# Performance work log

Hardware: AMD Instinct MI355X
Metric: run time of the kernel (lower is better)

Reference implementation:

```python
import jax, jax.numpy as jnp
import numpy as np
import math

NUM_CLASSES = 15
IN_CH = 256
FEAT_CH = 256
STRIDES = (8, 16, 32, 64, 128)
SCALES = (4.0,)
RATIOS = (6.0,)
ANGLES = (-0.125 * math.pi, 0.125 * math.pi, 0.375 * math.pi, 0.625 * math.pi)
NUM_ANCHORS = len(SCALES) * len(RATIOS) * len(ANGLES)  # 4
WH_RATIO_CLIP = 1e-6


def conv2d(x, w, b, pad):
    y = jax.lax.conv_general_dilated(
        x, w, window_strides=(1, 1), padding=[(pad, pad), (pad, pad)],
        dimension_numbers=("NCHW", "OIHW", "NCHW"))
    return y + b[None, :, None, None]


def gen_grid_anchors(base_size, feat_h, feat_w, stride):
    # AnchorGeneratorRotated (S2ANet style): base anchors [A,5] = (xc,yc,w,h,angle)
    scales = jnp.asarray(SCALES, jnp.float32)
    ratios = jnp.asarray(RATIOS, jnp.float32)
    angles = jnp.asarray(ANGLES, jnp.float32)
    h_ratios = jnp.sqrt(ratios)
    w_ratios = 1.0 / h_ratios
    ones = jnp.ones_like(angles)
    ws = (base_size * w_ratios[:, None, None] * scales[None, :, None] * ones[None, None, :]).reshape(-1)
    hs = (base_size * h_ratios[:, None, None] * scales[None, :, None] * ones[None, None, :]).reshape(-1)
    ang = jnp.tile(angles, ratios.size * scales.size)
    ctr = 0.5 * (base_size - 1.0)
    base = jnp.stack([jnp.full_like(ws, ctr), jnp.full_like(ws, ctr), ws, hs, ang], axis=-1)  # [A,5]
    xx = jnp.arange(feat_w, dtype=jnp.float32) * stride
    yy = jnp.arange(feat_h, dtype=jnp.float32) * stride
    gx, gy = jnp.meshgrid(xx, yy)  # [H,W]
    zeros = jnp.zeros_like(gx)
    shift = jnp.stack([gx, gy, zeros, zeros, zeros], axis=-1)  # [H,W,5]
    return base[None, None] + shift[:, :, None, :]  # [H,W,A,5]


def norm_angle(a):
    # normalize to [-pi/4, 3pi/4)
    return (a + 0.25 * jnp.pi) % jnp.pi - 0.25 * jnp.pi


def rboxes_decode(anchors, deltas):
    # is_encode_relative=False branch of delta2rbox
    max_ratio = abs(math.log(WH_RATIO_CLIP))
    dx, dy, dw, dh, da = jnp.split(deltas, 5, axis=-1)
    rx, ry, rw, rh, ra = jnp.split(anchors, 5, axis=-1)
    dw = jnp.clip(dw, -max_ratio, max_ratio)
    dh = jnp.clip(dh, -max_ratio, max_ratio)
    gx = dx * rw + rx
    gy = dy * rh + ry
    gw = rw * jnp.exp(dw)
    gh = rh * jnp.exp(dh)
    ga = norm_angle(da + ra)
    return jnp.concatenate([gx, gy, gw, gh, ga], axis=-1)


def _head_level(x, stride, p):
    B, _, H, W = x.shape
    # reg tower (2 stacked 3x3 conv + relu)
    r = jax.nn.relu(conv2d(x, p["reg_w0"], p["reg_b0"], 1))
    r = jax.nn.relu(conv2d(r, p["reg_w1"], p["reg_b1"], 1))
    bbox = conv2d(r, p["reg_head_w"], p["reg_head_b"], 0)
    bbox = bbox.transpose(0, 2, 3, 1).reshape(B, H, W, NUM_ANCHORS, 5)
    conf = conv2d(r, p["conf_w"], p["conf_b"], 0)
    conf = conf.transpose(0, 2, 3, 1).reshape(B, H, W, NUM_ANCHORS, 1)
    anchors = gen_grid_anchors(float(stride), H, W, float(stride))  # [H,W,A,5]
    dec = rboxes_decode(anchors[None], jax.lax.stop_gradient(bbox))  # [B,H,W,A,5]
    # refine-anchor selection: pick decoded box of max-confidence anchor per location
    conf_sig = jax.nn.sigmoid(jax.lax.stop_gradient(conf))[..., 0]  # [B,H,W,A]
    idx = jnp.argmax(conf_sig, axis=3)  # [B,H,W]
    refine = jnp.take_along_axis(dec, idx[..., None, None], axis=3)[:, :, :, 0, :]  # [B,H,W,5]
    # cls tower
    c = jax.nn.relu(conv2d(x, p["cls_w0"], p["cls_b0"], 1))
    c = jax.nn.relu(conv2d(c, p["cls_w1"], p["cls_b1"], 1))
    cls = conv2d(c, p["cls_head_w"], p["cls_head_b"], 0)
    cls = cls.transpose(0, 2, 3, 1).reshape(B, H, W, NUM_ANCHORS, NUM_CLASSES)
    # per-image scores as in get_bboxes: sigmoid(cls) * sigmoid(conf)
    scores = jax.nn.sigmoid(cls.reshape(B, -1, NUM_CLASSES)) * jax.nn.sigmoid(conf.reshape(B, -1, 1))
    return scores, dec.reshape(B, -1, 5), refine


def setup_inputs() -> dict:
    key = jax.random.key(0)
    ks = jax.random.split(key, 24)
    B = 8
    sizes = [(128, 128), (64, 64), (32, 32), (16, 16), (8, 8)]
    inp = {}
    for i, (h, w) in enumerate(sizes):
        inp[f"feat{i}"] = jax.random.normal(ks[i], (B, IN_CH, h, w), jnp.float32)
    std = 0.01
    bias_cls = float(-np.log((1 - 0.01) / 0.01))
    inp["reg_w0"] = jax.random.normal(ks[5], (FEAT_CH, IN_CH, 3, 3), jnp.float32) * std
    inp["reg_b0"] = jnp.zeros((FEAT_CH,), jnp.float32)
    inp["reg_w1"] = jax.random.normal(ks[6], (FEAT_CH, FEAT_CH, 3, 3), jnp.float32) * std
    inp["reg_b1"] = jnp.zeros((FEAT_CH,), jnp.float32)
    inp["cls_w0"] = jax.random.normal(ks[7], (FEAT_CH, IN_CH, 3, 3), jnp.float32) * std
    inp["cls_b0"] = jnp.zeros((FEAT_CH,), jnp.float32)
    inp["cls_w1"] = jax.random.normal(ks[8], (FEAT_CH, FEAT_CH, 3, 3), jnp.float32) * std
    inp["cls_b1"] = jnp.zeros((FEAT_CH,), jnp.float32)
    inp["reg_head_w"] = jax.random.normal(ks[9], (5 * NUM_ANCHORS, FEAT_CH, 1, 1), jnp.float32) * std
    inp["reg_head_b"] = jnp.zeros((5 * NUM_ANCHORS,), jnp.float32)
    inp["cls_head_w"] = jax.random.normal(ks[10], (NUM_CLASSES * NUM_ANCHORS, FEAT_CH, 1, 1), jnp.float32) * std
    inp["cls_head_b"] = jnp.full((NUM_CLASSES * NUM_ANCHORS,), bias_cls, jnp.float32)
    inp["conf_w"] = jax.random.normal(ks[11], (NUM_ANCHORS, FEAT_CH, 1, 1), jnp.float32) * std
    inp["conf_b"] = jnp.full((NUM_ANCHORS,), bias_cls, jnp.float32)
    return inp


def reference(feat0, feat1, feat2, feat3, feat4,
              reg_w0, reg_b0, reg_w1, reg_b1,
              cls_w0, cls_b0, cls_w1, cls_b1,
              reg_head_w, reg_head_b, cls_head_w, cls_head_b,
              conf_w, conf_b):
    p = dict(reg_w0=reg_w0, reg_b0=reg_b0, reg_w1=reg_w1, reg_b1=reg_b1,
             cls_w0=cls_w0, cls_b0=cls_b0, cls_w1=cls_w1, cls_b1=cls_b1,
             reg_head_w=reg_head_w, reg_head_b=reg_head_b,
             cls_head_w=cls_head_w, cls_head_b=cls_head_b,
             conf_w=conf_w, conf_b=conf_b)
    feats = [feat0, feat1, feat2, feat3, feat4]
    scores_ls, boxes_ls = [], []
    for x, s in zip(feats, STRIDES):
        sc, bx, _ = _head_level(x, s, p)
        scores_ls.append(sc)
        boxes_ls.append(bx)
    scores = jnp.concatenate(scores_ls, axis=1)  # [B, N_total, num_classes]
    boxes = jnp.concatenate(boxes_ls, axis=1)    # [B, N_total, 5]
    return scores, boxes
```

## Files before the change

kernel.cpp:

```cpp
#include <hip/hip_runtime.h>


typedef __attribute__((ext_vector_type(8))) _Float16 f16x8;
typedef __attribute__((ext_vector_type(4))) float f32x4;

#define SCORES_TOTAL 10475520ull

__device__ __forceinline__ unsigned short f2h(float f) {
  union { _Float16 h; unsigned short u; } x;
  x.h = (_Float16)f;
  return x.u;
}

__device__ __forceinline__ float sigmf(float x) {
  return 1.0f / (1.0f + expf(-x));
}

__device__ __forceinline__ void gload_lds16(const unsigned short* g,
                                            unsigned short* l) {
  __builtin_amdgcn_global_load_lds(
      (const __attribute__((address_space(1))) unsigned int*)g,
      (__attribute__((address_space(3))) unsigned int*)l, 16, 0, 0);
}

__device__ __forceinline__ void lvl_lookup(int gm, int& logW, int& mbase) {
  if (gm < 131072) { logW = 7; mbase = 0; }
  else if (gm < 163840) { logW = 6; mbase = 131072; }
  else if (gm < 172032) { logW = 5; mbase = 163840; }
  else if (gm < 174080) { logW = 4; mbase = 172032; }
  else { logW = 3; mbase = 174080; }
}

__global__ __launch_bounds__(256) void prep_convw(
    const float* __restrict__ w0, const float* __restrict__ w1,
    const float* __restrict__ w2, const float* __restrict__ w3,
    unsigned short* __restrict__ wtout) {
  int g = blockIdx.x * 256 + threadIdx.x;
  int q = g >> 16;
  int wsel = q / 9;
  int kk = q - wsel * 9;
  int r = g & 65535;
  int oc = r >> 8, ic = r & 255;
  const float* src = (wsel == 0) ? w0 : (wsel == 1) ? w1 : (wsel == 2) ? w2 : w3;
  float v = src[(size_t)(oc * 256 + ic) * 9 + kk];
  wtout[(size_t)wsel * 589824 + (size_t)((kk << 8) + oc) * 256 + ic] = f2h(v);
}

__global__ __launch_bounds__(256) void prep_small(
    const float* __restrict__ clsh, const float* __restrict__ regh,
    const float* __restrict__ confw,
    unsigned short* __restrict__ wc, unsigned short* __restrict__ wh,
    unsigned short* __restrict__ zp) {
  int g = blockIdx.x * 256 + threadIdx.x;
  if (g < 16384) {
    int row = g >> 8, ic = g & 255;
    float v = (row < 60) ? clsh[row * 256 + ic] : 0.0f;
    wc[g] = f2h(v);
  } else if (g < 24576) {
    int gg = g - 16384;
    int row = gg >> 8, ic = gg & 255;
    float v = 0.0f;
    if (row < 20) v = regh[row * 256 + ic];
    else if (row < 24) v = confw[(row - 20) * 256 + ic];
    wh[gg] = f2h(v);
  } else if (g < 24640) {
    zp[g - 24576] = 0;
  }
}

__global__ __launch_bounds__(256) void to_nhwc_all(
    const float* __restrict__ f0, const float* __restrict__ f1,
    const float* __restrict__ f2, const float* __restrict__ f3,
    const float* __restrict__ f4, unsigned short* __restrict__ out) {
  __shared__ unsigned short L[64][258];
  const int t = threadIdx.x;
  const int gm0 = blockIdx.x * 64;
  int logW, mbase;
  const float* in;
  if (gm0 < 131072) { logW = 7; mbase = 0; in = f0; }
  else if (gm0 < 163840) { logW = 6; mbase = 131072; in = f1; }
  else if (gm0 < 172032) { logW = 5; mbase = 163840; in = f2; }
  else if (gm0 < 174080) { logW = 4; mbase = 172032; in = f3; }
  else { logW = 3; mbase = 174080; in = f4; }
  const int logHW = 2 * logW;
  const int HW = 1 << logHW;
  const int lm0 = gm0 - mbase;
  const int b = lm0 >> logHW;
  const int hw0 = lm0 & (HW - 1);
#pragma unroll
  for (int it = 0; it < 16; ++it) {
    int c = it * 16 + (t >> 4);
    int j4 = (t & 15) * 4;
    float4 v = *reinterpret_cast<const float4*>(
        in + (size_t)(b * 256 + c) * HW + hw0 + j4);
    L[j4 + 0][c] = f2h(v.x);
    L[j4 + 1][c] = f2h(v.y);
    L[j4 + 2][c] = f2h(v.z);
    L[j4 + 3][c] = f2h(v.w);
  }
  __syncthreads();
#pragma unroll
  for (int it = 0; it < 16; ++it) {
    int j = it * 4 + (t >> 6);
    int c4 = (t & 63) * 4;
    unsigned v0 = (unsigned)L[j][c4 + 0] | ((unsigned)L[j][c4 + 1] << 16);
    unsigned v1 = (unsigned)L[j][c4 + 2] | ((unsigned)L[j][c4 + 3] << 16);
    uint2 v = make_uint2(v0, v1);
    *reinterpret_cast<uint2*>(out + ((size_t)(gm0 + j) << 8) + c4) = v;
  }
}

template <int LOGW>
__global__ __launch_bounds__(512, 2) void conv256p(
    const unsigned short* __restrict__ xin,
    const unsigned short* __restrict__ wt,
    const float* __restrict__ bias,
    const unsigned short* __restrict__ zp,
    unsigned short* __restrict__ yout,
    int gm_base) {
  __shared__ unsigned short pool[65536];
  const int t = threadIdx.x;
  const int lane = t & 63;
  const int wv = t >> 6;
  const int wm = wv >> 2;
  const int wn = wv & 3;
  const int gm0 = gm_base + blockIdx.x * 256;
  int logW, mbase;
  if constexpr (LOGW > 0) {
    logW = LOGW;
    mbase = 0;
  } else {
    lvl_lookup(gm0, logW, mbase);
  }
  const int H = 1 << logW, W = H;
  const int logHW = 2 * logW;
  const int HWm1 = (1 << logHW) - 1, Wm1 = W - 1;

  const int schk = ((lane & 3) ^ ((lane >> 3) & 3)) << 3;
  const unsigned short* aptr[2];
  const unsigned short* bptr[2];
  int amsk[2];
#pragma unroll
  for (int j = 0; j < 2; ++j) {
    int r = (wv << 5) + (j << 4) + (lane >> 2);
    int gm = gm0 + r;
    int lm = gm - mbase;
    int hw = lm & HWm1;
    int hj = hw >> logW, wj = hw & Wm1;
    aptr[j] = xin + ((size_t)gm << 8) + schk;
    bptr[j] = wt + ((size_t)r << 8) + schk;
    bool hm = hj > 0, hp = hj < H - 1, wlo = wj > 0, whi = wj < W - 1;
    int m = 0;
#pragma unroll
    for (int kk = 0; kk < 9; ++kk) {
      int dy = kk / 3 - 1, dxv = kk % 3 - 1;
      bool ok = (dy < 0 ? hm : (dy > 0 ? hp : true)) &&
                (dxv < 0 ? wlo : (dxv > 0 ? whi : true));
      m |= (ok ? 1 : 0) << kk;
    }
    amsk[j] = m;
  }
  const int sdstA = (wv << 10) + ((lane >> 6) << 9);

  f32x4 acc[8][4];
#pragma unroll
  for (int i = 0; i < 8; ++i)
#pragma unroll
    for (int j = 0; j < 4; ++j) acc[i][j] = (f32x4){0.f, 0.f, 0.f, 0.f};

  const int l15 = lane & 15;
  const int arow0 = (wm << 7) + l15;
  const int brow0 = (wn << 6) + l15;
  const int achk = (((lane >> 4) ^ ((lane >> 1) & 3)) << 4);

  {
    const int m0o = -((W + 1) << 8), m1o = -(W << 8), m2o = -((W - 1) << 8);
#pragma unroll
    for (int j = 0; j < 2; ++j) {
      const unsigned short* g0 = (amsk[j] & 1) ? (aptr[j] + m0o) : zp;
      gload_lds16(g0, pool + (wv << 10) + (j << 9));
      gload_lds16(bptr[j], pool + 32768 + (wv << 10) + (j << 9));
    }
#pragma unroll
    for (int j = 0; j < 2; ++j) {
      const unsigned short* g1 = ((amsk[j] >> 1) & 1) ? (aptr[j] + m1o) : zp;
      gload_lds16(g1, pool + 8192 + (wv << 10) + (j << 9));
      gload_lds16(bptr[j] + 65536, pool + 32768 + 8192 + (wv << 10) + (j << 9));
    }
#pragma unroll
    for (int j = 0; j < 2; ++j) {
      const unsigned short* g2 = ((amsk[j] >> 2) & 1) ? (aptr[j] + m2o) : zp;
      gload_lds16(g2, pool + 16384 + (wv << 10) + (j << 9));
      gload_lds16(bptr[j] + 131072,
                  pool + 32768 + 16384 + (wv << 10) + (j << 9));
    }
  }
  asm volatile("s_waitcnt vmcnt(8)" ::: "memory");
  __builtin_amdgcn_s_barrier();

  int kk3 = 3, ich3 = 0;
  int mo3 = -256;
  int bo3 = 3 << 16;

#pragma unroll 1
  for (int tt = 0; tt < 72; ++tt) {
    const int c = tt & 3;
    const int sb = (tt + 3) & 3;
    const bool st = (tt <= 68);
    const char* Ab = (const char*)pool + (c << 14);
    const char* Bb = (const char*)pool + 65536 + (c << 14);
    const int so = (ich3 << 5);
    f16x8 a[4], b[4];

#pragma unroll
    for (int mf = 0; mf < 4; ++mf)
      a[mf] = *reinterpret_cast<const f16x8*>(
          Ab + ((arow0 + (mf << 4)) << 6) + achk);
#pragma unroll
    for (int nf = 0; nf < 4; ++nf)
      b[nf] = *reinterpret_cast<const f16x8*>(
          Bb + ((brow0 + (nf << 4)) << 6) + achk);
    if (st) {
#pragma unroll
      for (int j = 0; j < 2; ++j) {
        const unsigned short* g =
            ((amsk[j] >> kk3) & 1) ? (aptr[j] + mo3 + so) : zp;
        gload_lds16(g, pool + (sb << 13) + (wv << 10) + (j << 9));
      }
    }
    __builtin_amdgcn_s_barrier();
    asm volatile("s_waitcnt lgkmcnt(0)" ::: "memory");
    __builtin_amdgcn_sched_barrier(0);
    __builtin_amdgcn_s_setprio(1);
#pragma unroll
    for (int mf = 0; mf < 4; ++mf)
#pragma unroll
      for (int nf = 0; nf < 4; ++nf)
        acc[mf][nf] = __builtin_amdgcn_mfma_f32_16x16x32_f16(
            a[mf], b[nf], acc[mf][nf], 0, 0, 0);
    __builtin_amdgcn_s_setprio(0);
    __builtin_amdgcn_s_barrier();

#pragma unroll
    for (int mf = 0; mf < 4; ++mf)
      a[mf] = *reinterpret_cast<const f16x8*>(
          Ab + ((arow0 + ((mf + 4) << 4)) << 6) + achk);
    if (st) {
#pragma unroll
      for (int j = 0; j < 2; ++j)
        gload_lds16(bptr[j] + bo3 + so,
                    pool + 32768 + (sb << 13) + (wv << 10) + (j << 9));
    }
    if (st) asm volatile("s_waitcnt vmcnt(8)" ::: "memory");
    else    asm volatile("s_waitcnt vmcnt(0)" ::: "memory");
    __builtin_amdgcn_s_barrier();
    asm volatile("s_waitcnt lgkmcnt(0)" ::: "memory");
    __builtin_amdgcn_sched_barrier(0);
    __builtin_amdgcn_s_setprio(1);
#pragma unroll
    for (int mf = 0; mf < 4; ++mf)
#pragma unroll
      for (int nf = 0; nf < 4; ++nf)
        acc[mf + 4][nf] = __builtin_amdgcn_mfma_f32_16x16x32_f16(
            a[mf], b[nf], acc[mf + 4][nf], 0, 0, 0);
    __builtin_amdgcn_s_setprio(0);
    __builtin_amdgcn_s_barrier();

    if (st) {
      kk3++;
      mo3 += 256;
      bo3 += 65536;
      if (kk3 == 9) {
        kk3 = 0;
        ich3++;
        mo3 = -((W + 1) << 8);
        bo3 = 0;
      } else if (kk3 == 3 || kk3 == 6) {
        mo3 += (W - 3) << 8;
      }
    }
  }
  __syncthreads();

  {
    const int eg = (lane >> 4) << 2;
    const int el = lane & 15;
#pragma unroll
    for (int nf = 0; nf < 4; ++nf) {
      float bi = bias[(wn << 6) + (nf << 4) + el];
#pragma unroll
      for (int mf = 0; mf < 8; ++mf)
#pragma unroll
        for (int r = 0; r < 4; ++r) {
          int wrow = (wm << 7) + (mf << 4) + eg + r;
          pool[(wrow << 8) + (wn << 6) + (nf << 4) + el] =
              f2h(fmaxf(acc[mf][nf][r] + bi, 0.0f));
        }
    }
  }
  __syncthreads();
  {
    const int row = t >> 1;
    const int half = t & 1;
    const unsigned short* src = pool + (row << 8) + (half << 7);
    unsigned short* dst = yout + ((size_t)(gm0 + row) << 8) + (half << 7);
#pragma unroll
    for (int q = 0; q < 16; ++q)
      reinterpret_cast<uint4*>(dst)[q] =
          reinterpret_cast<const uint4*>(src)[q];
  }
}

__global__ __launch_bounds__(256) void head24_mfma(
    const unsigned short* __restrict__ t2,
    const unsigned short* __restrict__ wh,
    const float* __restrict__ regb, const float* __restrict__ confb,
    float* __restrict__ hbuf) {
  const int t = threadIdx.x, lane = t & 63, wv = t >> 6;
  const int rowb = blockIdx.x * 256 + wv * 64;
  const int kgrp = (lane >> 4) << 3;
  const int l15 = lane & 15;
  f32x4 acc[4][2];
#pragma unroll
  for (int i = 0; i < 4; ++i)
#pragma unroll
    for (int j = 0; j < 2; ++j) acc[i][j] = (f32x4){0.f, 0.f, 0.f, 0.f};
#pragma unroll
  for (int k0 = 0; k0 < 256; k0 += 32) {
    f16x8 a[4], b[2];
#pragma unroll
    for (int mf = 0; mf < 4; ++mf)
      a[mf] = *reinterpret_cast<const f16x8*>(
          t2 + (((size_t)(rowb + (mf << 4) + l15)) << 8) + k0 + kgrp);
#pragma unroll
    for (int nf = 0; nf < 2; ++nf)
      b[nf] = *reinterpret_cast<const f16x8*>(
          wh + (size_t)(((nf << 4) + l15) << 8) + k0 + kgrp);
#pragma unroll
    for (int mf = 0; mf < 4; ++mf)
#pragma unroll
      for (int nf = 0; nf < 2; ++nf)
        acc[mf][nf] = __builtin_amdgcn_mfma_f32_16x16x32_f16(
            a[mf], b[nf], acc[mf][nf], 0, 0, 0);
  }
#pragma unroll
  for (int nf = 0; nf < 2; ++nf) {
    int c = (nf << 4) + l15;
    if (c < 24) {
      float bi = (c < 20) ? regb[c] : confb[c - 20];
#pragma unroll
      for (int mf = 0; mf < 4; ++mf)
#pragma unroll
        for (int r = 0; r < 4; ++r) {
          int m = rowb + (mf << 4) + ((lane >> 4) << 2) + r;
          hbuf[(size_t)m * 24 + c] = acc[mf][nf][r] + bi;
        }
    }
  }
}

__global__ __launch_bounds__(256) void cls_scores(
    const unsigned short* __restrict__ t2,
    const unsigned short* __restrict__ wcw,
    const float* __restrict__ clsb,
    const float* __restrict__ hbuf,
    float* __restrict__ outs, int gm_base) {
  const int t = threadIdx.x, lane = t & 63, wv = t >> 6;
  const int gm0 = gm_base + blockIdx.x * 256;
  int logW, mbase, lvl_off;
  if (gm0 < 131072) { logW = 7; mbase = 0; lvl_off = 0; }
  else if (gm0 < 163840) { logW = 6; mbase = 131072; lvl_off = 65536; }
  else if (gm0 < 172032) { logW = 5; mbase = 163840; lvl_off = 81920; }
  else if (gm0 < 174080) { logW = 4; mbase = 172032; lvl_off = 86016; }
  else { logW = 3; mbase = 174080; lvl_off = 87040; }
  const int logHW = 2 * logW, HWm1 = (1 << logHW) - 1;
  const int rowb = gm0 + wv * 64;
  const int kgrp = (lane >> 4) << 3;
  const int l15 = lane & 15;
  f32x4 acc[4][4];
#pragma unroll
  for (int i = 0; i < 4; ++i)
#pragma unroll
    for (int j = 0; j < 4; ++j) acc[i][j] = (f32x4){0.f, 0.f, 0.f, 0.f};
#pragma unroll
  for (int k0 = 0; k0 < 256; k0 += 32) {
    f16x8 a[4], b[4];
#pragma unroll
    for (int mf = 0; mf < 4; ++mf)
      a[mf] = *reinterpret_cast<const f16x8*>(
          t2 + (((size_t)(rowb + (mf << 4) + l15)) << 8) + k0 + kgrp);
#pragma unroll
    for (int nf = 0; nf < 4; ++nf)
      b[nf] = *reinterpret_cast<const f16x8*>(
          wcw + (size_t)(((nf << 4) + l15) << 8) + k0 + kgrp);
#pragma unroll
    for (int mf = 0; mf < 4; ++mf)
#pragma unroll
      for (int nf = 0; nf < 4; ++nf)
        acc[mf][nf] = __builtin_amdgcn_mfma_f32_16x16x32_f16(
            a[mf], b[nf], acc[mf][nf], 0, 0, 0);
  }
#pragma unroll
  for (int nf = 0; nf < 4; ++nf) {
    int c = (nf << 4) + l15;
    if (c < 60) {
      int ai = c / 15, ci = c - ai * 15;
      float bi = clsb[c];
#pragma unroll
      for (int mf = 0; mf < 4; ++mf)
#pragma unroll
        for (int r = 0; r < 4; ++r) {
          int m = rowb + (mf << 4) + ((lane >> 4) << 2) + r;
          float logit = acc[mf][nf][r] + bi;
          float conf = hbuf[(size_t)m * 24 + 20 + ai];
          float sc = sigmf(logit) * sigmf(conf);
          int lm = m - mbase;
          int b = lm >> logHW;
          int hw = lm & HWm1;
          int loc = lvl_off + (hw << 2) + ai;
          outs[(size_t)b * 1309440 + (size_t)loc * 15 + ci] = sc;
        }
    }
  }
}

__global__ __launch_bounds__(256) void decode_all(
    const float* __restrict__ hbuf, float* __restrict__ outb) {
  int tid = blockIdx.x * 256 + threadIdx.x;
  if (tid >= 174592 * 4) return;
  int m = tid >> 2, a = tid & 3;
  int logW, mbase, lvl_off;
  float stride;
  if (m < 131072) { logW = 7; mbase = 0; lvl_off = 0; stride = 8.f; }
  else if (m < 163840) { logW = 6; mbase = 131072; lvl_off = 65536; stride = 16.f; }
  else if (m < 172032) { logW = 5; mbase = 163840; lvl_off = 81920; stride = 32.f; }
  else if (m < 174080) { logW = 4; mbase = 172032; lvl_off = 86016; stride = 64.f; }
  else { logW = 3; mbase = 174080; lvl_off = 87040; stride = 128.f; }
  const int logHW = 2 * logW;
  const float ANG[4] = {-0.39269908169872414f, 0.39269908169872414f,
                        1.1780972450961724f, 1.9634954084936207f};
  const float* d = hbuf + (size_t)m * 24 + a * 5;
  float dx = d[0], dy = d[1], dw = d[2], dh = d[3], da = d[4];
  int lm = m - mbase;
  int b = lm >> logHW, hw = lm & ((1 << logHW) - 1);
  int h = hw >> logW, w = hw & ((1 << logW) - 1);
  float ctr = 0.5f * (stride - 1.0f);
  float rx = w * stride + ctr, ry = h * stride + ctr;
  float rw = stride * 1.6329931618554521f;
  float rh = stride * 9.7979589711327124f;
  const float MR = 13.815510557964274f;
  dw = fminf(fmaxf(dw, -MR), MR);
  dh = fminf(fmaxf(dh, -MR), MR);
  float gx = dx * rw + rx;
  float gy = dy * rh + ry;
  float gw = rw * expf(dw);
  float gh = rh * expf(dh);
  float v = da + ANG[a] + 0.7853981633974483f;
  float r = fmodf(v, 3.14159265358979323846f);
  if (r < 0.0f) r += 3.14159265358979323846f;
  float ga = r - 0.7853981633974483f;
  int loc = lvl_off + (hw << 2) + a;
  size_t base = (size_t)b * 436480 + (size_t)loc * 5;
  outb[base + 0] = gx;
  outb[base + 1] = gy;
  outb[base + 2] = gw;
  outb[base + 3] = gh;
  outb[base + 4] = ga;
}

extern "C" void kernel_launch(void* const* d_in, const int* in_sizes, int n_in,
                              void* d_out, int out_size, void* d_ws,
                              size_t ws_size, hipStream_t stream) {
  const float* feats[5];
  for (int i = 0; i < 5; ++i) feats[i] = (const float*)d_in[i];
  const float* reg_w0 = (const float*)d_in[5];
  const float* reg_b0 = (const float*)d_in[6];
  const float* reg_w1 = (const float*)d_in[7];
  const float* reg_b1 = (const float*)d_in[8];
  const float* cls_w0 = (const float*)d_in[9];
  const float* cls_b0 = (const float*)d_in[10];
  const float* cls_w1 = (const float*)d_in[11];
  const float* cls_b1 = (const float*)d_in[12];
  const float* reg_head_w = (const float*)d_in[13];
  const float* reg_head_b = (const float*)d_in[14];
  const float* cls_head_w = (const float*)d_in[15];
  const float* cls_head_b = (const float*)d_in[16];
  const float* conf_w = (const float*)d_in[17];
  const float* conf_b = (const float*)d_in[18];

  unsigned short* ws = (unsigned short*)d_ws;
  unsigned short* t1r = ws + 44695552ull;
  unsigned short* t1c = ws + 78249984ull;
  unsigned short* wt4 = ws + 111804416ull;
  unsigned short* wh = ws + 114163712ull;
  unsigned short* wc = ws + 114171904ull;
  unsigned short* zp = ws + 114188288ull;
  float* hbuf_all = (float*)((char*)d_ws + 228376704ull);

  prep_convw<<<9216, 256, 0, stream>>>(reg_w0, reg_w1, cls_w0, cls_w1, wt4);
  prep_small<<<97, 256, 0, stream>>>(cls_head_w, reg_head_w, conf_w, wc, wh,
                                     zp);
  to_nhwc_all<<<2728, 256, 0, stream>>>(feats[0], feats[1], feats[2], feats[3],
                                        feats[4], ws);

  float* scores = (float*)d_out;
  float* boxes = (float*)d_out + SCORES_TOTAL;

  static const int g_base[2] = {0, 131072};
  static const int g_M[2] = {131072, 43520};
  for (int g = 0; g < 2; ++g) {
    const int base = g_base[g];
    const int M = g_M[g];
    const int nb = M / 256;
    const size_t bofs = ((size_t)base << 8);
    unsigned short* t1r_v = t1r - bofs;
    unsigned short* t1c_v = t1c - bofs;
    if (g == 0) {
      conv256p<7><<<nb, 512, 0, stream>>>(ws, wt4 + 0ull * 589824, reg_b0, zp,
                                          t1r_v, base);
      conv256p<7><<<nb, 512, 0, stream>>>(ws, wt4 + 2ull * 589824, cls_b0, zp,
                                          t1c_v, base);
      conv256p<7><<<nb, 512, 0, stream>>>(t1r_v, wt4 + 1ull * 589824, reg_b1,
                                          zp, ws, base);
    } else {
      conv256p<0><<<nb, 512, 0, stream>>>(ws, wt4 + 0ull * 589824, reg_b0, zp,
                                          t1r_v, base);
      conv256p<0><<<nb, 512, 0, stream>>>(ws, wt4 + 2ull * 589824, cls_b0, zp,
                                          t1c_v, base);
      conv256p<0><<<nb, 512, 0, stream>>>(t1r_v, wt4 + 1ull * 589824, reg_b1,
                                          zp, ws, base);
    }
    head24_mfma<<<nb, 256, 0, stream>>>(ws + bofs, wh, reg_head_b, conf_b,
                                        hbuf_all + (size_t)base * 24);
    if (g == 0)
      conv256p<7><<<nb, 512, 0, stream>>>(t1c_v, wt4 + 3ull * 589824, cls_b1,
                                          zp, ws, base);
    else
      conv256p<0><<<nb, 512, 0, stream>>>(t1c_v, wt4 + 3ull * 589824, cls_b1,
                                          zp, ws, base);
    cls_scores<<<nb, 256, 0, stream>>>(ws, wc, cls_head_b, hbuf_all, scores,
                                       base);
  }
  decode_all<<<(174592 * 4 + 255) / 256, 256, 0, stream>>>(hbuf_all, boxes);
}
```

Measured before the change: 1.155 ms.

## Restructure conv main loop with inline-asm LDS reads and merge first-layer convs

Rewrites the implicit-GEMM conv inner loop to issue all twelve LDS fragment reads up front through inline ds_read_b128 with immediate offsets. It uses a single barrier per K-step and splits the waits (lgkmcnt(4), then lgkmcnt(0)) so the first half of the MFMAs can start while the B/A reads for the second half are still in flight. The two first-layer convs (reg and cls) that read the same input are merged into one launch using blockIdx.y, which doubles the grid and removes a launch. The templated compile-time level width is dropped in favour of a runtime lookup. The reduced barriers and the hand-placed waitcnts carry a risk of LDS hazards.

```diff
diff --git a/kernel.cpp b/kernel.cpp
--- a/kernel.cpp
+++ b/kernel.cpp
@@ -22,6 +22,13 @@
       (const __attribute__((address_space(1))) unsigned int*)g,
       (__attribute__((address_space(3))) unsigned int*)l, 16, 0, 0);
 }
+
+__device__ __forceinline__ unsigned lds_addr(const void* p) {
+  return (unsigned)(size_t)(const __attribute__((address_space(3))) char*)p;
+}
+
+#define DSR(d, va, off) \
+  asm volatile("ds_read_b128 %0, %1 offset:" off : "=v"(d) : "v"(va))
 
 __device__ __forceinline__ void lvl_lookup(int gm, int& logW, int& mbase) {
   if (gm < 131072) { logW = 7; mbase = 0; }
@@ -110,15 +117,20 @@
   }
 }
 
-template <int LOGW>
-__global__ __launch_bounds__(512, 2) void conv256p(
+__global__ __launch_bounds__(512, 2) void conv256q(
     const unsigned short* __restrict__ xin,
-    const unsigned short* __restrict__ wt,
-    const float* __restrict__ bias,
+    const unsigned short* __restrict__ wtA,
+    const unsigned short* __restrict__ wtB,
+    const float* __restrict__ biasA, const float* __restrict__ biasB,
     const unsigned short* __restrict__ zp,
-    unsigned short* __restrict__ yout,
+    unsigned short* __restrict__ outA, unsigned short* __restrict__ outB,
     int gm_base) {
   __shared__ unsigned short pool[65536];
+  const int sel = blockIdx.y;
+  const unsigned short* wt = sel ? wtB : wtA;
+  const float* bias = sel ? biasB : biasA;
+  unsigned short* yout = sel ? outB : outA;
+
   const int t = threadIdx.x;
   const int lane = t & 63;
   const int wv = t >> 6;
@@ -126,12 +138,7 @@
   const int wn = wv & 3;
   const int gm0 = gm_base + blockIdx.x * 256;
   int logW, mbase;
-  if constexpr (LOGW > 0) {
-    logW = LOGW;
-    mbase = 0;
-  } else {
-    lvl_lookup(gm0, logW, mbase);
-  }
+  lvl_lookup(gm0, logW, mbase);
   const int H = 1 << logW, W = H;
   const int logHW = 2 * logW;
   const int HWm1 = (1 << logHW) - 1, Wm1 = W - 1;
@@ -160,7 +167,7 @@
     }
     amsk[j] = m;
   }
-  const int sdstA = (wv << 10) + ((lane >> 6) << 9);
+  const int sdst = ((wv << 5) << 5);
 
   f32x4 acc[8][4];
 #pragma unroll
@@ -172,113 +179,128 @@
   const int arow0 = (wm << 7) + l15;
   const int brow0 = (wn << 6) + l15;
   const int achk = (((lane >> 4) ^ ((lane >> 1) & 3)) << 4);
+  const unsigned pbase = lds_addr(pool);
+  const unsigned abase = pbase + (arow0 << 6) + achk;
+  const unsigned bbase = pbase + 65536 + (brow0 << 6) + achk;
 
   {
     const int m0o = -((W + 1) << 8), m1o = -(W << 8), m2o = -((W - 1) << 8);
 #pragma unroll
     for (int j = 0; j < 2; ++j) {
-      const unsigned short* g0 = (amsk[j] & 1) ? (aptr[j] + m0o) : zp;
-      gload_lds16(g0, pool + (wv << 10) + (j << 9));
-      gload_lds16(bptr[j], pool + 32768 + (wv << 10) + (j << 9));
+      gload_lds16((amsk[j] & 1) ? (aptr[j] + m0o) : zp,
+                  pool + sdst + (j << 9));
+      gload_lds16(bptr[j], pool + 32768 + sdst + (j << 9));
     }
 #pragma unroll
     for (int j = 0; j < 2; ++j) {
-      const unsigned short* g1 = ((amsk[j] >> 1) & 1) ? (aptr[j] + m1o) : zp;
-      gload_lds16(g1, pool + 8192 + (wv << 10) + (j << 9));
-      gload_lds16(bptr[j] + 65536, pool + 32768 + 8192 + (wv << 10) + (j << 9));
+      gload_lds16(((amsk[j] >> 1) & 1) ? (aptr[j] + m1o) : zp,
+                  pool + 8192 + sdst + (j << 9));
+      gload_lds16(bptr[j] + 65536, pool + 32768 + 8192 + sdst + (j << 9));
     }
 #pragma unroll
     for (int j = 0; j < 2; ++j) {
-      const unsigned short* g2 = ((amsk[j] >> 2) & 1) ? (aptr[j] + m2o) : zp;
-      gload_lds16(g2, pool + 16384 + (wv << 10) + (j << 9));
-      gload_lds16(bptr[j] + 131072,
-                  pool + 32768 + 16384 + (wv << 10) + (j << 9));
-    }
-  }
-  asm volatile("s_waitcnt vmcnt(8)" ::: "memory");
-  __builtin_amdgcn_s_barrier();
-
-  int kk3 = 3, ich3 = 0;
+      gload_lds16(((amsk[j] >> 2) & 1) ? (aptr[j] + m2o) : zp,
+                  pool + 16384 + sdst + (j << 9));
+      gload_lds16(bptr[j] + 131072, pool + 32768 + 16384 + sdst + (j << 9));
+    }
+  }
+  asm volatile("s_waitcnt vmcnt(8)");
+
+  int kk3 = 3;
   int mo3 = -256;
   int bo3 = 3 << 16;
+  int so3 = 0;
 
 #pragma unroll 1
   for (int tt = 0; tt < 72; ++tt) {
+    __builtin_amdgcn_s_barrier();
     const int c = tt & 3;
     const int sb = (tt + 3) & 3;
-    const bool st = (tt <= 68);
-    const char* Ab = (const char*)pool + (c << 14);
-    const char* Bb = (const char*)pool + 65536 + (c << 14);
-    const int so = (ich3 << 5);
-    f16x8 a[4], b[4];
-
-#pragma unroll
-    for (int mf = 0; mf < 4; ++mf)
-      a[mf] = *reinterpret_cast<const f16x8*>(
-          Ab + ((arow0 + (mf << 4)) << 6) + achk);
-#pragma unroll
-    for (int nf = 0; nf < 4; ++nf)
-      b[nf] = *reinterpret_cast<const f16x8*>(
-          Bb + ((brow0 + (nf << 4)) << 6) + achk);
-    if (st) {
+    const unsigned ava = abase + (c << 14);
+    const unsigned bva = bbase + (c << 14);
+    f16x8 a0, a1, a2, a3, a4, a5, a6, a7, b0, b1, b2, b3;
+
+    DSR(a0, ava, "0");
+    DSR(a1, ava, "1024");
+    DSR(a2, ava, "2048");
+    DSR(a3, ava, "3072");
+    DSR(b0, bva, "0");
+    DSR(b1, bva, "1024");
+    DSR(b2, bva, "2048");
+    DSR(b3, bva, "3072");
+    DSR(a4, ava, "4096");
+    DSR(a5, ava, "5120");
+    DSR(a6, ava, "6144");
+    DSR(a7, ava, "7168");
+    if (tt < 69) {
 #pragma unroll
       for (int j = 0; j < 2; ++j) {
         const unsigned short* g =
-            ((amsk[j] >> kk3) & 1) ? (aptr[j] + mo3 + so) : zp;
-        gload_lds16(g, pool + (sb << 13) + (wv << 10) + (j << 9));
+            ((amsk[j] >> kk3) & 1) ? (aptr[j] + mo3 + so3) : zp;
+        gload_lds16(g, pool + (sb << 13) + sdst + (j << 9));
       }
-    }
-    __builtin_amdgcn_s_barrier();
-    asm volatile("s_waitcnt lgkmcnt(0)" ::: "memory");
-    __builtin_amdgcn_sched_barrier(0);
-    __builtin_amdgcn_s_setprio(1);
-#pragma unroll
-    for (int mf = 0; mf < 4; ++mf)
-#pragma unroll
-      for (int nf = 0; nf < 4; ++nf)
-        acc[mf][nf] = __builtin_amdgcn_mfma_f32_16x16x32_f16(
-            a[mf], b[nf], acc[mf][nf], 0, 0, 0);
-    __builtin_amdgcn_s_setprio(0);
-    __builtin_amdgcn_s_barrier();
-
-#pragma unroll
-    for (int mf = 0; mf < 4; ++mf)
-      a[mf] = *reinterpret_cast<const f16x8*>(
-          Ab + ((arow0 + ((mf + 4) << 4)) << 6) + achk);
-    if (st) {
 #pragma unroll
       for (int j = 0; j < 2; ++j)
-        gload_lds16(bptr[j] + bo3 + so,
-                    pool + 32768 + (sb << 13) + (wv << 10) + (j << 9));
-    }
-    if (st) asm volatile("s_waitcnt vmcnt(8)" ::: "memory");
-    else    asm volatile("s_waitcnt vmcnt(0)" ::: "memory");
-    __builtin_amdgcn_s_barrier();
-    asm volatile("s_waitcnt lgkmcnt(0)" ::: "memory");
-    __builtin_amdgcn_sched_barrier(0);
-    __builtin_amdgcn_s_setprio(1);
-#pragma unroll
-    for (int mf = 0; mf < 4; ++mf)
-#pragma unroll
-      for (int nf = 0; nf < 4; ++nf)
-        acc[mf + 4][nf] = __builtin_amdgcn_mfma_f32_16x16x32_f16(
-            a[mf], b[nf], acc[mf + 4][nf], 0, 0, 0);
-    __builtin_amdgcn_s_setprio(0);
-    __builtin_amdgcn_s_barrier();
-
-    if (st) {
+        gload_lds16(bptr[j] + bo3 + so3,
+                    pool + 32768 + (sb << 13) + sdst + (j << 9));
       kk3++;
       mo3 += 256;
       bo3 += 65536;
       if (kk3 == 9) {
         kk3 = 0;
-        ich3++;
+        so3 += 32;
         mo3 = -((W + 1) << 8);
         bo3 = 0;
       } else if (kk3 == 3 || kk3 == 6) {
         mo3 += (W - 3) << 8;
       }
     }
+
+    asm volatile("s_waitcnt lgkmcnt(4)");
+    __builtin_amdgcn_sched_barrier(0);
+    __builtin_amdgcn_s_setprio(1);
+    acc[0][0] = __builtin_amdgcn_mfma_f32_16x16x32_f16(a0, b0, acc[0][0], 0, 0, 0);
+    acc[0][1] = __builtin_amdgcn_mfma_f32_16x16x32_f16(a0, b1, acc[0][1], 0, 0, 0);
+    acc[0][2] = __builtin_amdgcn_mfma_f32_16x16x32_f16(a0, b2, acc[0][2], 0, 0, 0);
+    acc[0][3] = __builtin_amdgcn_mfma_f32_16x16x32_f16(a0, b3, acc[0][3], 0, 0, 0);
+    acc[1][0] = __builtin_amdgcn_mfma_f32_16x16x32_f16(a1, b0, acc[1][0], 0, 0, 0);
+    acc[1][1] = __builtin_amdgcn_mfma_f32_16x16x32_f16(a1, b1, acc[1][1], 0, 0, 0);
+    acc[1][2] = __builtin_amdgcn_mfma_f32_16x16x32_f16(a1, b2, acc[1][2], 0, 0, 0);
+    acc[1][3] = __builtin_amdgcn_mfma_f32_16x16x32_f16(a1, b3, acc[1][3], 0, 0, 0);
+    acc[2][0] = __builtin_amdgcn_mfma_f32_16x16x32_f16(a2, b0, acc[2][0], 0, 0, 0);
+    acc[2][1] = __builtin_amdgcn_mfma_f32_16x16x32_f16(a2, b1, acc[2][1], 0, 0, 0);
+    acc[2][2] = __builtin_amdgcn_mfma_f32_16x16x32_f16(a2, b2, acc[2][2], 0, 0, 0);
+    acc[2][3] = __builtin_amdgcn_mfma_f32_16x16x32_f16(a2, b3, acc[2][3], 0, 0, 0);
+    acc[3][0] = __builtin_amdgcn_mfma_f32_16x16x32_f16(a3, b0, acc[3][0], 0, 0, 0);
+    acc[3][1] = __builtin_amdgcn_mfma_f32_16x16x32_f16(a3, b1, acc[3][1], 0, 0, 0);
+    acc[3][2] = __builtin_amdgcn_mfma_f32_16x16x32_f16(a3, b2, acc[3][2], 0, 0, 0);
+    acc[3][3] = __builtin_amdgcn_mfma_f32_16x16x32_f16(a3, b3, acc[3][3], 0, 0, 0);
+    __builtin_amdgcn_s_setprio(0);
+
+    asm volatile("s_waitcnt lgkmcnt(0)");
+    __builtin_amdgcn_sched_barrier(0);
+    __builtin_amdgcn_s_setprio(1);
+    acc[4][0] = __builtin_amdgcn_mfma_f32_16x16x32_f16(a4, b0, acc[4][0], 0, 0, 0);
+    acc[4][1] = __builtin_amdgcn_mfma_f32_16x16x32_f16(a4, b1, acc[4][1], 0, 0, 0);
+    acc[4][2] = __builtin_amdgcn_mfma_f32_16x16x32_f16(a4, b2, acc[4][2], 0, 0, 0);
+    acc[4][3] = __builtin_amdgcn_mfma_f32_16x16x32_f16(a4, b3, acc[4][3], 0, 0, 0);
+    acc[5][0] = __builtin_amdgcn_mfma_f32_16x16x32_f16(a5, b0, acc[5][0], 0, 0, 0);
+    acc[5][1] = __builtin_amdgcn_mfma_f32_16x16x32_f16(a5, b1, acc[5][1], 0, 0, 0);
+    acc[5][2] = __builtin_amdgcn_mfma_f32_16x16x32_f16(a5, b2, acc[5][2], 0, 0, 0);
+    acc[5][3] = __builtin_amdgcn_mfma_f32_16x16x32_f16(a5, b3, acc[5][3], 0, 0, 0);
+    acc[6][0] = __builtin_amdgcn_mfma_f32_16x16x32_f16(a6, b0, acc[6][0], 0, 0, 0);
+    acc[6][1] = __builtin_amdgcn_mfma_f32_16x16x32_f16(a6, b1, acc[6][1], 0, 0, 0);
+    acc[6][2] = __builtin_amdgcn_mfma_f32_16x16x32_f16(a6, b2, acc[6][2], 0, 0, 0);
+    acc[6][3] = __builtin_amdgcn_mfma_f32_16x16x32_f16(a6, b3, acc[6][3], 0, 0, 0);
+    acc[7][0] = __builtin_amdgcn_mfma_f32_16x16x32_f16(a7, b0, acc[7][0], 0, 0, 0);
+    acc[7][1] = __builtin_amdgcn_mfma_f32_16x16x32_f16(a7, b1, acc[7][1], 0, 0, 0);
+    acc[7][2] = __builtin_amdgcn_mfma_f32_16x16x32_f16(a7, b2, acc[7][2], 0, 0, 0);
+    acc[7][3] = __builtin_amdgcn_mfma_f32_16x16x32_f16(a7, b3, acc[7][3], 0, 0, 0);
+    __builtin_amdgcn_s_setprio(0);
+
+    if (tt < 69)      asm volatile("s_waitcnt vmcnt(8)");
+    else if (tt == 69) asm volatile("s_waitcnt vmcnt(4)");
+    else               asm volatile("s_waitcnt vmcnt(0)");
   }
   __syncthreads();
 
@@ -506,38 +528,26 @@
   float* scores = (float*)d_out;
   float* boxes = (float*)d_out + SCORES_TOTAL;
 
-  static const int g_base[2] = {0, 131072};
-  static const int g_M[2] = {131072, 43520};
+  static const int gbase[2] = {0, 131072};
+  static const int gM[2] = {131072, 43520};
   for (int g = 0; g < 2; ++g) {
-    const int base = g_base[g];
-    const int M = g_M[g];
+    const int base = gbase[g];
+    const int M = gM[g];
     const int nb = M / 256;
     const size_t bofs = ((size_t)base << 8);
     unsigned short* t1r_v = t1r - bofs;
     unsigned short* t1c_v = t1c - bofs;
-    if (g == 0) {
-      conv256p<7><<<nb, 512, 0, stream>>>(ws, wt4 + 0ull * 589824, reg_b0, zp,
-                                          t1r_v, base);
-      conv256p<7><<<nb, 512, 0, stream>>>(ws, wt4 + 2ull * 589824, cls_b0, zp,
-                                          t1c_v, base);
-      conv256p<7><<<nb, 512, 0, stream>>>(t1r_v, wt4 + 1ull * 589824, reg_b1,
-                                          zp, ws, base);
-    } else {
-      conv256p<0><<<nb, 512, 0, stream>>>(ws, wt4 + 0ull * 589824, reg_b0, zp,
-                                          t1r_v, base);
-      conv256p<0><<<nb, 512, 0, stream>>>(ws, wt4 + 2ull * 589824, cls_b0, zp,
-                                          t1c_v, base);
-      conv256p<0><<<nb, 512, 0, stream>>>(t1r_v, wt4 + 1ull * 589824, reg_b1,
-                                          zp, ws, base);
-    }
+    conv256q<<<dim3(nb, 2), 512, 0, stream>>>(
+        ws, wt4 + 0ull * 589824, wt4 + 2ull * 589824, reg_b0, cls_b0, zp,
+        t1r_v, t1c_v, base);
+    conv256q<<<dim3(nb, 1), 512, 0, stream>>>(
+        t1r_v, wt4 + 1ull * 589824, wt4 + 1ull * 589824, reg_b1, reg_b1, zp,
+        ws, ws, base);
     head24_mfma<<<nb, 256, 0, stream>>>(ws + bofs, wh, reg_head_b, conf_b,
                                         hbuf_all + (size_t)base * 24);
-    if (g == 0)
-      conv256p<7><<<nb, 512, 0, stream>>>(t1c_v, wt4 + 3ull * 589824, cls_b1,
-                                          zp, ws, base);
-    else
-      conv256p<0><<<nb, 512, 0, stream>>>(t1c_v, wt4 + 3ull * 589824, cls_b1,
-                                          zp, ws, base);
+    conv256q<<<dim3(nb, 1), 512, 0, stream>>>(
+        t1c_v, wt4 + 3ull * 589824, wt4 + 3ull * 589824, cls_b1, cls_b1, zp,
+        ws, ws, base);
     cls_scores<<<nb, 256, 0, stream>>>(ws, wc, cls_head_b, hbuf_all, scores,
                                        base);
   }
```

After: 1.111 ms. 3.8% less time.
